# Kernel optimization log

Measured on AMD Instinct MI355X. Metric: run time of the kernel, lower is better.

## Reference

```python
import jax, jax.numpy as jnp
import numpy as np

EMB_DIM = 1024
NUM_HEADS = 16
HEAD_DIM = EMB_DIM // NUM_HEADS


def _theta_vector(head_dim):
    # theta_i = 10000^(-2i/head_dim), i = 0..head_dim/2-1 (standard RoPE)
    i = jnp.arange(head_dim // 2, dtype=jnp.float32)
    return jnp.power(10000.0, -2.0 * i / head_dim)


def _apply_rope(x, cos, sin):
    # x: [B,S,H,D]; cos,sin: [B,S,1,D/2]. Pairwise 2x2 rotation per dim-pair.
    B, S, H, D = x.shape
    xp = x.reshape(B, S, H, D // 2, 2)
    x0, x1 = xp[..., 0], xp[..., 1]
    r0 = x0 * cos - x1 * sin
    r1 = x0 * sin + x1 * cos
    return jnp.stack([r0, r1], axis=-1).reshape(B, S, H, D)


def setup_inputs() -> dict:
    key = jax.random.key(0)
    ks = jax.random.split(key, 11)
    B, S = 2, 2048
    sc = 1.0 / np.sqrt(EMB_DIM)
    x = jax.random.normal(ks[0], (B, S, EMB_DIM), dtype=jnp.float32)
    positions = jnp.sort(jax.random.randint(ks[1], (B, S), 0, 8192), axis=-1)
    Wq = jax.random.normal(ks[2], (EMB_DIM, EMB_DIM), dtype=jnp.float32) * sc
    bq = jax.random.normal(ks[3], (EMB_DIM,), dtype=jnp.float32) * 0.01
    Wk = jax.random.normal(ks[4], (EMB_DIM, EMB_DIM), dtype=jnp.float32) * sc
    bk = jax.random.normal(ks[5], (EMB_DIM,), dtype=jnp.float32) * 0.01
    Wv = jax.random.normal(ks[6], (EMB_DIM, EMB_DIM), dtype=jnp.float32) * sc
    bv = jax.random.normal(ks[7], (EMB_DIM,), dtype=jnp.float32) * 0.01
    Wo = jax.random.normal(ks[8], (EMB_DIM, EMB_DIM), dtype=jnp.float32) * sc
    bo = jax.random.normal(ks[9], (EMB_DIM,), dtype=jnp.float32) * 0.01
    return {"x": x, "positions": positions, "Wq": Wq, "bq": bq, "Wk": Wk,
            "bk": bk, "Wv": Wv, "bv": bv, "Wo": Wo, "bo": bo}


def reference(x, positions, Wq, bq, Wk, bk, Wv, bv, Wo, bo):
    B, S, E = x.shape
    H, D = NUM_HEADS, HEAD_DIM
    Q = (x @ Wq + bq).reshape(B, S, H, D)
    K = (x @ Wk + bk).reshape(B, S, H, D)
    V = (x @ Wv + bv).reshape(B, S, H, D)
    theta = _theta_vector(D)                       # [D/2]
    ang = positions.astype(jnp.float32)[..., None] * theta  # [B,S,D/2]
    cos = jnp.cos(ang)[:, :, None, :]              # [B,S,1,D/2]
    sin = jnp.sin(ang)[:, :, None, :]
    Qr = _apply_rope(Q, cos, sin).transpose(0, 2, 1, 3)   # [B,H,S,D]
    Kr = _apply_rope(K, cos, sin).transpose(0, 2, 1, 3)
    Vh = V.transpose(0, 2, 1, 3)
    scores = jnp.einsum('bhqd,bhkd->bhqk', Qr, Kr) / jnp.sqrt(jnp.float32(D))
    probs = jax.nn.softmax(scores, axis=-1)
    ctx = jnp.einsum('bhqk,bhkd->bhqd', probs, Vh)
    ctx = ctx.transpose(0, 2, 1, 3).reshape(B, S, E)
    return ctx @ Wo + bo
```

## Files before the change

kernel.cpp:

```cpp
#include <hip/hip_runtime.h>
#include <hip/hip_bf16.h>
#include <math.h>

#define B_ 2
#define S_ 2048
#define E_ 1024
#define H_ 16
#define D_ 64
#define M_ 4096
#define NT2 32
#define KVB 64

typedef __bf16 bf16;
typedef __bf16 bf16x4 __attribute__((ext_vector_type(4)));
typedef __bf16 bf16x8 __attribute__((ext_vector_type(8)));
typedef float f32x4 __attribute__((ext_vector_type(4)));
typedef float f32x16 __attribute__((ext_vector_type(16)));

__device__ __forceinline__ void gload_lds16(const void* g, void* lds) {
  __builtin_amdgcn_global_load_lds(
      (const __attribute__((address_space(1))) unsigned int*)g,
      (__attribute__((address_space(3))) unsigned int*)lds, 16, 0, 0);
}

#define MFMA16(a, b, c) __builtin_amdgcn_mfma_f32_16x16x32_bf16(a, b, c, 0, 0, 0)
#define MFMA32(a, b, c) __builtin_amdgcn_mfma_f32_32x32x16_bf16(a, b, c, 0, 0, 0)

__global__ __launch_bounds__(256)
void split_f32_kernel(const float* __restrict__ in, bf16* __restrict__ hi,
                      bf16* __restrict__ lo, int n4) {
  int i = blockIdx.x * 256 + threadIdx.x;
  if (i >= n4) return;
  float4 v = ((const float4*)in)[i];
  bf16 h0 = (bf16)v.x, h1 = (bf16)v.y, h2 = (bf16)v.z, h3 = (bf16)v.w;
  bf16x4 hv = {h0, h1, h2, h3};
  bf16x4 lv = {(bf16)(v.x - (float)h0), (bf16)(v.y - (float)h1),
               (bf16)(v.z - (float)h2), (bf16)(v.w - (float)h3)};
  *(bf16x4*)(hi + 4 * (size_t)i) = hv;
  *(bf16x4*)(lo + 4 * (size_t)i) = lv;
}

__global__ __launch_bounds__(256)
void transpose_split4_kernel(const float* __restrict__ Wq, const float* __restrict__ Wk,
                             const float* __restrict__ Wv, const float* __restrict__ Wo,
                             bf16* __restrict__ Tqh, bf16* __restrict__ Tql,
                             bf16* __restrict__ Tkh, bf16* __restrict__ Tkl,
                             bf16* __restrict__ Tvh, bf16* __restrict__ Tvl,
                             bf16* __restrict__ Toh, bf16* __restrict__ Tol) {
  const int z = blockIdx.z;
  const float* W = z == 0 ? Wq : z == 1 ? Wk : z == 2 ? Wv : Wo;
  bf16* Th = z == 0 ? Tqh : z == 1 ? Tkh : z == 2 ? Tvh : Toh;
  bf16* Tl = z == 0 ? Tql : z == 1 ? Tkl : z == 2 ? Tvl : Tol;
  __shared__ float tile[32][33];
  const int tx = threadIdx.x & 31, ty = threadIdx.x >> 5;
  const int c0 = blockIdx.x * 32, r0 = blockIdx.y * 32;
#pragma unroll
  for (int i = 0; i < 4; ++i)
    tile[ty + 8 * i][tx] = W[(size_t)(r0 + ty + 8 * i) * E_ + c0 + tx];
  __syncthreads();
#pragma unroll
  for (int i = 0; i < 4; ++i) {
    int rr = ty + 8 * i;
    float v = tile[tx][rr];
    bf16 hv = (bf16)v;
    size_t oidx = (size_t)(c0 + rr) * E_ + r0 + tx;
    Th[oidx] = hv;
    Tl[oidx] = (bf16)(v - (float)hv);
  }
}

__global__ __launch_bounds__(256)
void rope_tab_kernel(const int* __restrict__ pos, float* __restrict__ cosT,
                     float* __restrict__ sinT) {
  int idx = blockIdx.x * 256 + threadIdx.x;
  int t = idx & 31, bs = idx >> 5;
  double th = pow(10000.0, -(double)(2 * t) / 64.0);
  float ang = (float)pos[bs] * (float)th;
  double a = (double)ang;
  cosT[idx] = (float)cos(a);
  sinT[idx] = (float)sin(a);
}

#define BMg 128
#define BNg 128
#define BKg 32

__global__ __launch_bounds__(512, 4)
void gemm_qkv_kernel(const bf16* __restrict__ Ah_g, const bf16* __restrict__ Al_g,
                     const bf16* __restrict__ BhQ, const bf16* __restrict__ BlQ,
                     const bf16* __restrict__ BhK, const bf16* __restrict__ BlK,
                     const bf16* __restrict__ BhV, const bf16* __restrict__ BlV,
                     const float* __restrict__ bqp, const float* __restrict__ bkp,
                     const float* __restrict__ bvp,
                     const float* __restrict__ cosT, const float* __restrict__ sinT,
                     bf16* __restrict__ Qh, bf16* __restrict__ Qlo,
                     bf16* __restrict__ Kh, bf16* __restrict__ Klo,
                     bf16* __restrict__ VTb) {
  __shared__ bf16 lA[BMg * 64];
  __shared__ bf16 lB[BNg * 64];
  const int tid = threadIdx.x;
  const int nb = blockIdx.x;
  const int third = nb >> 3;
  const int n0 = (nb & 7) * BNg;
  const int m0 = blockIdx.y * BMg;
  const bf16* Bh_g = third == 0 ? BhQ : third == 1 ? BhK : BhV;
  const bf16* Bl_g = third == 0 ? BlQ : third == 1 ? BlK : BlV;
  const float* bias = third == 0 ? bqp : third == 1 ? bkp : bvp;
  const int wave = tid >> 6, lane = tid & 63;
  const int wr = wave >> 2, wc = wave & 3;
  const int r = lane & 31, half = lane >> 5;
  const int KD = 1024;

  f32x16 acc[2] = {};

  for (int kt = 0; kt < KD / BKg; ++kt) {
    const int k0 = kt * BKg;
    {
#pragma unroll
      for (int i = 0; i < 2; ++i) {
        int c = i * 512 + tid;
        int row = c >> 3, u = c & 7;
        int us = u ^ (row & 7);
        int uu = us & 3;
        char* lpA = (char*)lA + (size_t)(i * 512 + wave * 64) * 16;
        char* lpB = (char*)lB + (size_t)(i * 512 + wave * 64) * 16;
        const bf16* sA = (us < 4) ? Ah_g : Al_g;
        const bf16* sB = (us < 4) ? Bh_g : Bl_g;
        gload_lds16((const char*)(sA + (size_t)(m0 + row) * KD + k0) + uu * 16,
                    lpA);
        gload_lds16((const char*)(sB + (size_t)(n0 + row) * KD + k0) + uu * 16,
                    lpB);
      }
    }
    __syncthreads();
#pragma unroll
    for (int ks = 0; ks < 2; ++ks) {
      bf16x8 a_h[2], a_l[2], b_h, b_l;
#pragma unroll
      for (int mi = 0; mi < 2; ++mi) {
        int row = wr * 64 + mi * 32 + r;
        int sw = (row & 7) << 4;
        const char* base = (const char*)lA + row * 128;
        a_h[mi] = *(const bf16x8*)(base + ((ks * 32 + half * 16) ^ sw));
        a_l[mi] = *(const bf16x8*)(base + ((64 + ks * 32 + half * 16) ^ sw));
      }
      {
        int row = wc * 32 + r;
        int sw = (row & 7) << 4;
        const char* base = (const char*)lB + row * 128;
        b_h = *(const bf16x8*)(base + ((ks * 32 + half * 16) ^ sw));
        b_l = *(const bf16x8*)(base + ((64 + ks * 32 + half * 16) ^ sw));
      }
      __builtin_amdgcn_s_setprio(1);
#pragma unroll
      for (int mi = 0; mi < 2; ++mi) {
        acc[mi] = MFMA32(a_h[mi], b_h, acc[mi]);
        acc[mi] = MFMA32(a_h[mi], b_l, acc[mi]);
        acc[mi] = MFMA32(a_l[mi], b_h, acc[mi]);
      }
      __builtin_amdgcn_s_setprio(0);
    }
    __syncthreads();
  }

#pragma unroll
  for (int mi = 0; mi < 2; ++mi) {
    const int gcol = n0 + wc * 32 + r;
    const float bv = bias[gcol];
    if (third < 2) {
      bf16* outH = third == 0 ? Qh : Kh;
      bf16* outL = third == 0 ? Qlo : Klo;
      const int h = gcol >> 6, d = gcol & 63, tt = d >> 1;
#pragma unroll
      for (int tq = 0; tq < 4; ++tq) {
#pragma unroll
        for (int u = 0; u < 4; ++u) {
          int reg = tq * 4 + u;
          int grow = m0 + wr * 64 + mi * 32 + (u + 8 * tq + 4 * half);
          int s = grow & (S_ - 1), b = grow >> 11;
          float v = acc[mi][reg] + bv;
          float other = __shfl_xor(v, 1);
          float cs = cosT[(size_t)(b * S_ + s) * NT2 + tt];
          float sn = sinT[(size_t)(b * S_ + s) * NT2 + tt];
          float vr = (d & 1) ? (other * sn + v * cs) : (v * cs - other * sn);
          if (third == 0) vr *= 0.125f;
          bf16 hv = (bf16)vr;
          bf16 lv = (bf16)(vr - (float)hv);
          size_t idx = (((size_t)(b * H_ + h)) * S_ + s) * D_ + d;
          outH[idx] = hv;
          outL[idx] = lv;
        }
      }
    } else {
      const int h = gcol >> 6, d = gcol & 63;
#pragma unroll
      for (int tq = 0; tq < 4; ++tq) {
        int grow = m0 + wr * 64 + mi * 32 + (8 * tq + 4 * half);
        int s = grow & (S_ - 1), b = grow >> 11;
        ushort4 pk;
        unsigned short* pp = (unsigned short*)&pk;
#pragma unroll
        for (int u = 0; u < 4; ++u) {
          float v = acc[mi][tq * 4 + u] + bv;
          bf16 hv = (bf16)v;
          pp[u] = __builtin_bit_cast(unsigned short, hv);
        }
        *(ushort4*)((unsigned short*)VTb +
                    (((size_t)(b * H_ + h)) * D_ + d) * S_ + s) = pk;
      }
    }
  }
}

__global__ __launch_bounds__(512, 4)
void gemm_o_kernel(const bf16* __restrict__ Ah_g, const bf16* __restrict__ Al_g,
                   const bf16* __restrict__ Bh_g, const bf16* __restrict__ Bl_g,
                   const float* __restrict__ bias, float* __restrict__ outF) {
  __shared__ bf16 lA[BMg * 64];
  __shared__ bf16 lB[BNg * 64];
  const int tid = threadIdx.x;
  const int m0 = blockIdx.y * BMg, n0 = blockIdx.x * BNg;
  const int wave = tid >> 6, lane = tid & 63;
  const int wr = wave >> 2, wc = wave & 3;
  const int r = lane & 31, half = lane >> 5;
  const int KD = 1024;

  f32x16 acc[2] = {};

  for (int kt = 0; kt < KD / BKg; ++kt) {
    const int k0 = kt * BKg;
    {
#pragma unroll
      for (int i = 0; i < 2; ++i) {
        int c = i * 512 + tid;
        int row = c >> 3, u = c & 7;
        int us = u ^ (row & 7);
        int uu = us & 3;
        char* lpA = (char*)lA + (size_t)(i * 512 + wave * 64) * 16;
        char* lpB = (char*)lB + (size_t)(i * 512 + wave * 64) * 16;
        const bf16* sA = (us < 4) ? Ah_g : Al_g;
        const bf16* sB = (us < 4) ? Bh_g : Bl_g;
        gload_lds16((const char*)(sA + (size_t)(m0 + row) * KD + k0) + uu * 16,
                    lpA);
        gload_lds16((const char*)(sB + (size_t)(n0 + row) * KD + k0) + uu * 16,
                    lpB);
      }
    }
    __syncthreads();
#pragma unroll
    for (int ks = 0; ks < 2; ++ks) {
      bf16x8 a_h[2], a_l[2], b_h, b_l;
#pragma unroll
      for (int mi = 0; mi < 2; ++mi) {
        int row = wr * 64 + mi * 32 + r;
        int sw = (row & 7) << 4;
        const char* base = (const char*)lA + row * 128;
        a_h[mi] = *(const bf16x8*)(base + ((ks * 32 + half * 16) ^ sw));
        a_l[mi] = *(const bf16x8*)(base + ((64 + ks * 32 + half * 16) ^ sw));
      }
      {
        int row = wc * 32 + r;
        int sw = (row & 7) << 4;
        const char* base = (const char*)lB + row * 128;
        b_h = *(const bf16x8*)(base + ((ks * 32 + half * 16) ^ sw));
        b_l = *(const bf16x8*)(base + ((64 + ks * 32 + half * 16) ^ sw));
      }
      __builtin_amdgcn_s_setprio(1);
#pragma unroll
      for (int mi = 0; mi < 2; ++mi) {
        acc[mi] = MFMA32(a_h[mi], b_h, acc[mi]);
        acc[mi] = MFMA32(a_h[mi], b_l, acc[mi]);
        acc[mi] = MFMA32(a_l[mi], b_h, acc[mi]);
      }
      __builtin_amdgcn_s_setprio(0);
    }
    __syncthreads();
  }

#pragma unroll
  for (int mi = 0; mi < 2; ++mi) {
    const int gcol = n0 + wc * 32 + r;
    const float bv = bias[gcol];
#pragma unroll
    for (int tq = 0; tq < 4; ++tq)
#pragma unroll
      for (int u = 0; u < 4; ++u) {
        int grow = m0 + wr * 64 + mi * 32 + (u + 8 * tq + 4 * half);
        outF[(size_t)grow * E_ + gcol] = acc[mi][tq * 4 + u] + bv;
      }
  }
}

__global__ __launch_bounds__(256)
void attn_kernel(const bf16* __restrict__ Qh, const bf16* __restrict__ Ql,
                 const bf16* __restrict__ Kh, const bf16* __restrict__ Kl,
                 const bf16* __restrict__ VT, bf16* __restrict__ Ch,
                 bf16* __restrict__ Cl) {
  __shared__ bf16 sKh[2][KVB * 64];
  __shared__ bf16 sKl[2][KVB * 64];
  __shared__ bf16 sV[2][KVB * 64];

  const int tid = threadIdx.x;
  const int wave = tid >> 6, lane = tid & 63;
  const int r = lane & 15, hq = lane >> 4;
  const int bid = blockIdx.x;
  const int swz = (bid & 7) * 64 + (bid >> 3);
  const int bh = swz >> 4, qblk = swz & 15;
  const int q0 = qblk * 128 + wave * 32;
  const size_t hb = (size_t)bh * (S_ * D_);
  const size_t vb = (size_t)bh * (D_ * S_);

  bf16x8 qh[2][2], ql[2][2];
#pragma unroll
  for (int mi = 0; mi < 2; ++mi)
#pragma unroll
    for (int ks = 0; ks < 2; ++ks) {
      size_t off = hb + (size_t)(q0 + mi * 16 + r) * D_ + ks * 32 + hq * 8;
      qh[mi][ks] = *(const bf16x8*)&Qh[off];
      ql[mi][ks] = *(const bf16x8*)&Ql[off];
    }

  float m_lane[2] = {-1e30f, -1e30f};
  float l_lane[2] = {0.f, 0.f};
  f32x4 o[2][4] = {};

  auto stageK = [&](int kt, int buf) {
    const bf16* kbh = Kh + hb + (size_t)kt * (KVB * D_);
    const bf16* kbl = Kl + hb + (size_t)kt * (KVB * D_);
#pragma unroll
    for (int i = 0; i < 2; ++i) {
      int c = i * 256 + tid;
      int ldo = (i * 256 + wave * 64) * 16;
      int cs = c ^ ((c >> 3) & 7);
      gload_lds16(kbh + cs * 8, (char*)&sKh[buf][0] + ldo);
      gload_lds16(kbl + cs * 8, (char*)&sKl[buf][0] + ldo);
    }
  };
  uint4 vld[2];
  auto loadV = [&](int kt) {
    const bf16* vbp = VT + vb + kt * KVB;
#pragma unroll
    for (int i = 0; i < 2; ++i) {
      int c = i * 256 + tid;
      int row = c >> 3, w = c & 7;
      vld[i] = *(const uint4*)(vbp + (size_t)row * S_ + w * 8);
    }
  };
  auto writeV = [&](int buf) {
#pragma unroll
    for (int i = 0; i < 2; ++i) {
      int c = i * 256 + tid;
      int row = c >> 3, w = c & 7;
      int pb0 = (w >> 2) * 32 + (w & 1) * 16 + ((w >> 1) & 1) * 4;
      char* base = (char*)&sV[buf][0] + row * 128;
      uint2 lo = {vld[i].x, vld[i].y};
      uint2 hi = {vld[i].z, vld[i].w};
      *(uint2*)(base + ((pb0 * 2) ^ ((row & 7) << 4))) = lo;
      *(uint2*)(base + (((pb0 + 8) * 2) ^ ((row & 7) << 4))) = hi;
    }
  };

  stageK(0, 0);
  loadV(0);
  writeV(0);
  __syncthreads();
  int cur = 0;

  for (int kt = 0; kt < S_ / KVB; ++kt) {
    if (kt + 1 < S_ / KVB) {
      stageK(kt + 1, cur ^ 1);
      loadV(kt + 1);
    }

    f32x4 sf[2][4] = {};
#pragma unroll
    for (int nf = 0; nf < 4; ++nf)
#pragma unroll
      for (int ks = 0; ks < 2; ++ks) {
        int kk = nf * 16 + r;
        int boff = (kk * 128 + ks * 64 + hq * 16) ^ ((kk & 7) << 4);
        bf16x8 kkh = *(const bf16x8*)((const char*)&sKh[cur][0] + boff);
        bf16x8 kkl = *(const bf16x8*)((const char*)&sKl[cur][0] + boff);
#pragma unroll
        for (int mi = 0; mi < 2; ++mi) {
          sf[mi][nf] = MFMA16(kkh, qh[mi][ks], sf[mi][nf]);
          sf[mi][nf] = MFMA16(kkh, ql[mi][ks], sf[mi][nf]);
          sf[mi][nf] = MFMA16(kkl, qh[mi][ks], sf[mi][nf]);
        }
      }

    float lmax[2];
#pragma unroll
    for (int mi = 0; mi < 2; ++mi) {
      f32x4 m4;
#pragma unroll
      for (int e = 0; e < 4; ++e)
        m4[e] = fmaxf(fmaxf(sf[mi][0][e], sf[mi][1][e]),
                      fmaxf(sf[mi][2][e], sf[mi][3][e]));
      lmax[mi] = fmaxf(fmaxf(m4[0], m4[1]), fmaxf(m4[2], m4[3]));
    }
    int need = (lmax[0] > m_lane[0] + 8.f) || (lmax[1] > m_lane[1] + 8.f);
    if (__any(need)) {
#pragma unroll
      for (int mi = 0; mi < 2; ++mi) {
        float mx = lmax[mi];
        mx = fmaxf(mx, __shfl_xor(mx, 16));
        mx = fmaxf(mx, __shfl_xor(mx, 32));
        float mn = fmaxf(m_lane[mi], mx);
        float al = __expf(m_lane[mi] - mn);
        l_lane[mi] *= al;
        m_lane[mi] = mn;
        int alb = __builtin_bit_cast(int, al);
#pragma unroll
        for (int j = 0; j < 4; ++j) {
          int g = __builtin_amdgcn_ds_bpermute((hq * 4 + j) * 4, alb);
          float a = __builtin_bit_cast(float, g);
#pragma unroll
          for (int nd = 0; nd < 4; ++nd) o[mi][nd][j] *= a;
        }
      }
    }
    bf16x8 pa[2][2];
#pragma unroll
    for (int mi = 0; mi < 2; ++mi) {
      f32x4 s4 = {};
#pragma unroll
      for (int nf = 0; nf < 4; ++nf)
#pragma unroll
        for (int e = 0; e < 4; ++e) {
          float pv = __expf(sf[mi][nf][e] - m_lane[mi]);
          sf[mi][nf][e] = pv;
          s4[e] += pv;
        }
      l_lane[mi] += s4[0] + s4[1] + s4[2] + s4[3];
#pragma unroll
      for (int ks = 0; ks < 2; ++ks) {
        bf16x8 t;
#pragma unroll
        for (int e = 0; e < 4; ++e) {
          t[e] = (bf16)sf[mi][2 * ks][e];
          t[4 + e] = (bf16)sf[mi][2 * ks + 1][e];
        }
        pa[mi][ks] = t;
      }
    }

#pragma unroll
    for (int nd = 0; nd < 4; ++nd)
#pragma unroll
      for (int ks = 0; ks < 2; ++ks) {
        int dd = nd * 16 + r;
        int boff = (dd * 128 + ks * 64 + hq * 16) ^ ((dd & 7) << 4);
        bf16x8 vv = *(const bf16x8*)((const char*)&sV[cur][0] + boff);
#pragma unroll
        for (int mi = 0; mi < 2; ++mi)
          o[mi][nd] = MFMA16(pa[mi][ks], vv, o[mi][nd]);
      }

    if (kt + 1 < S_ / KVB) writeV(cur ^ 1);
    __syncthreads();
    cur ^= 1;
  }

  const int b = bh >> 4, h = bh & 15;
  float lq[2][4];
#pragma unroll
  for (int mi = 0; mi < 2; ++mi) {
    float lr = l_lane[mi];
    lr += __shfl_xor(lr, 16);
    lr += __shfl_xor(lr, 32);
    int lb = __builtin_bit_cast(int, lr);
#pragma unroll
    for (int j = 0; j < 4; ++j) {
      int g = __builtin_amdgcn_ds_bpermute((hq * 4 + j) * 4, lb);
      lq[mi][j] = __builtin_bit_cast(float, g);
    }
  }
#pragma unroll
  for (int mi = 0; mi < 2; ++mi)
#pragma unroll
    for (int nd = 0; nd < 4; ++nd)
#pragma unroll
      for (int j = 0; j < 4; ++j) {
        int s = q0 + mi * 16 + hq * 4 + j;
        int d = nd * 16 + r;
        float ov = o[mi][nd][j] / lq[mi][j];
        bf16 hv = (bf16)ov;
        bf16 lv = (bf16)(ov - (float)hv);
        size_t idx = (((size_t)(b * S_ + s)) * H_ + h) * D_ + d;
        Ch[idx] = hv;
        Cl[idx] = lv;
      }
}

extern "C" void kernel_launch(void* const* d_in, const int* in_sizes, int n_in,
                              void* d_out, int out_size, void* d_ws, size_t ws_size,
                              hipStream_t stream) {
  const float* x = (const float*)d_in[0];
  const int* pos = (const int*)d_in[1];
  const float* Wq = (const float*)d_in[2];
  const float* bq = (const float*)d_in[3];
  const float* Wk = (const float*)d_in[4];
  const float* bk = (const float*)d_in[5];
  const float* Wv = (const float*)d_in[6];
  const float* bv = (const float*)d_in[7];
  const float* Wo = (const float*)d_in[8];
  const float* bo = (const float*)d_in[9];
  float* out = (float*)d_out;

  char* p = (char*)d_ws;
  auto alloc = [&](size_t bytes) {
    char* rp = p;
    p += (bytes + 255) & ~(size_t)255;
    return rp;
  };
  const size_t XB = (size_t)M_ * E_ * sizeof(bf16);
  const size_t WB = (size_t)E_ * E_ * sizeof(bf16);
  const size_t TB = (size_t)B_ * S_ * NT2 * sizeof(float);
  bf16* Xh = (bf16*)alloc(XB);
  bf16* Xl = (bf16*)alloc(XB);
  bf16* WqTh = (bf16*)alloc(WB); bf16* WqTl = (bf16*)alloc(WB);
  bf16* WkTh = (bf16*)alloc(WB); bf16* WkTl = (bf16*)alloc(WB);
  bf16* WvTh = (bf16*)alloc(WB); bf16* WvTl = (bf16*)alloc(WB);
  bf16* WoTh = (bf16*)alloc(WB); bf16* WoTl = (bf16*)alloc(WB);
  float* cosT = (float*)alloc(TB);
  float* sinT = (float*)alloc(TB);
  bf16* Qh = (bf16*)alloc(XB); bf16* Qlo = (bf16*)alloc(XB);
  bf16* Kh = (bf16*)alloc(XB); bf16* Klo = (bf16*)alloc(XB);
  bf16* VTb = (bf16*)alloc(XB);
  bf16* Ch = Xh;
  bf16* Cl = Xl;

  split_f32_kernel<<<M_ * E_ / 4 / 256, 256, 0, stream>>>(x, Xh, Xl, M_ * E_ / 4);
  dim3 tg(32, 32, 4);
  transpose_split4_kernel<<<tg, 256, 0, stream>>>(Wq, Wk, Wv, Wo, WqTh, WqTl,
                                                  WkTh, WkTl, WvTh, WvTl, WoTh,
                                                  WoTl);
  rope_tab_kernel<<<B_ * S_ * NT2 / 256, 256, 0, stream>>>(pos, cosT, sinT);

  dim3 gq(24, 32);
  gemm_qkv_kernel<<<gq, 512, 0, stream>>>(Xh, Xl, WqTh, WqTl, WkTh, WkTl, WvTh,
                                          WvTl, bq, bk, bv, cosT, sinT, Qh, Qlo,
                                          Kh, Klo, VTb);

  attn_kernel<<<B_ * H_ * (S_ / 128), 256, 0, stream>>>(Qh, Qlo, Kh, Klo, VTb,
                                                        Ch, Cl);

  dim3 go(8, 32);
  gemm_o_kernel<<<go, 512, 0, stream>>>(Ch, Cl, WoTh, WoTl, bo, out);
}
```

Measured before the change: 237.7 us.

## Merge prep kernels, split MFMA accumulators, retile output projection GEMM

Fuses the x split, weight transpose/split and RoPE table kernels into a single launch with block-range dispatch, which removes two kernel launches and their gaps. In both GEMMs the low-part correction MFMA now accumulates into a second accumulator, which breaks the serial dependency chain so consecutive MFMAs can issue back to back. The output projection GEMM moves to 64x128 tiles with 256 threads and twice as many blocks, improving occupancy across CUs. This costs extra accumulator registers and changes the summation order slightly.

```diff
diff --git a/kernel.cpp b/kernel.cpp
--- a/kernel.cpp
+++ b/kernel.cpp
@@ -27,58 +27,57 @@
 #define MFMA32(a, b, c) __builtin_amdgcn_mfma_f32_32x32x16_bf16(a, b, c, 0, 0, 0)
 
 __global__ __launch_bounds__(256)
-void split_f32_kernel(const float* __restrict__ in, bf16* __restrict__ hi,
-                      bf16* __restrict__ lo, int n4) {
-  int i = blockIdx.x * 256 + threadIdx.x;
-  if (i >= n4) return;
-  float4 v = ((const float4*)in)[i];
-  bf16 h0 = (bf16)v.x, h1 = (bf16)v.y, h2 = (bf16)v.z, h3 = (bf16)v.w;
-  bf16x4 hv = {h0, h1, h2, h3};
-  bf16x4 lv = {(bf16)(v.x - (float)h0), (bf16)(v.y - (float)h1),
-               (bf16)(v.z - (float)h2), (bf16)(v.w - (float)h3)};
-  *(bf16x4*)(hi + 4 * (size_t)i) = hv;
-  *(bf16x4*)(lo + 4 * (size_t)i) = lv;
-}
-
-__global__ __launch_bounds__(256)
-void transpose_split4_kernel(const float* __restrict__ Wq, const float* __restrict__ Wk,
-                             const float* __restrict__ Wv, const float* __restrict__ Wo,
-                             bf16* __restrict__ Tqh, bf16* __restrict__ Tql,
-                             bf16* __restrict__ Tkh, bf16* __restrict__ Tkl,
-                             bf16* __restrict__ Tvh, bf16* __restrict__ Tvl,
-                             bf16* __restrict__ Toh, bf16* __restrict__ Tol) {
-  const int z = blockIdx.z;
-  const float* W = z == 0 ? Wq : z == 1 ? Wk : z == 2 ? Wv : Wo;
-  bf16* Th = z == 0 ? Tqh : z == 1 ? Tkh : z == 2 ? Tvh : Toh;
-  bf16* Tl = z == 0 ? Tql : z == 1 ? Tkl : z == 2 ? Tvl : Tol;
-  __shared__ float tile[32][33];
-  const int tx = threadIdx.x & 31, ty = threadIdx.x >> 5;
-  const int c0 = blockIdx.x * 32, r0 = blockIdx.y * 32;
-#pragma unroll
-  for (int i = 0; i < 4; ++i)
-    tile[ty + 8 * i][tx] = W[(size_t)(r0 + ty + 8 * i) * E_ + c0 + tx];
-  __syncthreads();
-#pragma unroll
-  for (int i = 0; i < 4; ++i) {
-    int rr = ty + 8 * i;
-    float v = tile[tx][rr];
-    bf16 hv = (bf16)v;
-    size_t oidx = (size_t)(c0 + rr) * E_ + r0 + tx;
-    Th[oidx] = hv;
-    Tl[oidx] = (bf16)(v - (float)hv);
-  }
-}
-
-__global__ __launch_bounds__(256)
-void rope_tab_kernel(const int* __restrict__ pos, float* __restrict__ cosT,
-                     float* __restrict__ sinT) {
-  int idx = blockIdx.x * 256 + threadIdx.x;
-  int t = idx & 31, bs = idx >> 5;
-  double th = pow(10000.0, -(double)(2 * t) / 64.0);
-  float ang = (float)pos[bs] * (float)th;
-  double a = (double)ang;
-  cosT[idx] = (float)cos(a);
-  sinT[idx] = (float)sin(a);
+void prep_kernel(const float* __restrict__ x, const int* __restrict__ pos,
+                 const float* __restrict__ Wq, const float* __restrict__ Wk,
+                 const float* __restrict__ Wv, const float* __restrict__ Wo,
+                 bf16* __restrict__ Xh, bf16* __restrict__ Xl,
+                 bf16* __restrict__ Tqh, bf16* __restrict__ Tql,
+                 bf16* __restrict__ Tkh, bf16* __restrict__ Tkl,
+                 bf16* __restrict__ Tvh, bf16* __restrict__ Tvl,
+                 bf16* __restrict__ Toh, bf16* __restrict__ Tol,
+                 float* __restrict__ cosT, float* __restrict__ sinT) {
+  const int bid = blockIdx.x;
+  if (bid < 4096) {
+    int i = bid * 256 + threadIdx.x;
+    float4 v = ((const float4*)x)[i];
+    bf16 h0 = (bf16)v.x, h1 = (bf16)v.y, h2 = (bf16)v.z, h3 = (bf16)v.w;
+    bf16x4 hv = {h0, h1, h2, h3};
+    bf16x4 lv = {(bf16)(v.x - (float)h0), (bf16)(v.y - (float)h1),
+                 (bf16)(v.z - (float)h2), (bf16)(v.w - (float)h3)};
+    *(bf16x4*)(Xh + 4 * (size_t)i) = hv;
+    *(bf16x4*)(Xl + 4 * (size_t)i) = lv;
+  } else if (bid < 8192) {
+    int t = bid - 4096;
+    int z = t >> 10, rem = t & 1023;
+    int bx = rem & 31, by = rem >> 5;
+    const float* W = z == 0 ? Wq : z == 1 ? Wk : z == 2 ? Wv : Wo;
+    bf16* Th = z == 0 ? Tqh : z == 1 ? Tkh : z == 2 ? Tvh : Toh;
+    bf16* Tl = z == 0 ? Tql : z == 1 ? Tkl : z == 2 ? Tvl : Tol;
+    __shared__ float tile[32][33];
+    const int tx = threadIdx.x & 31, ty = threadIdx.x >> 5;
+    const int c0 = bx * 32, r0 = by * 32;
+#pragma unroll
+    for (int i = 0; i < 4; ++i)
+      tile[ty + 8 * i][tx] = W[(size_t)(r0 + ty + 8 * i) * E_ + c0 + tx];
+    __syncthreads();
+#pragma unroll
+    for (int i = 0; i < 4; ++i) {
+      int rr = ty + 8 * i;
+      float v = tile[tx][rr];
+      bf16 hv = (bf16)v;
+      size_t oidx = (size_t)(c0 + rr) * E_ + r0 + tx;
+      Th[oidx] = hv;
+      Tl[oidx] = (bf16)(v - (float)hv);
+    }
+  } else {
+    int idx = (bid - 8192) * 256 + threadIdx.x;
+    int t = idx & 31, bs = idx >> 5;
+    double th = pow(10000.0, -(double)(2 * t) / 64.0);
+    float ang = (float)pos[bs] * (float)th;
+    double a = (double)ang;
+    cosT[idx] = (float)cos(a);
+    sinT[idx] = (float)sin(a);
+  }
 }
 
 #define BMg 128
@@ -112,6 +111,7 @@
   const int KD = 1024;
 
   f32x16 acc[2] = {};
+  f32x16 acc2[2] = {};
 
   for (int kt = 0; kt < KD / BKg; ++kt) {
     const int k0 = kt * BKg;
@@ -156,7 +156,7 @@
       for (int mi = 0; mi < 2; ++mi) {
         acc[mi] = MFMA32(a_h[mi], b_h, acc[mi]);
         acc[mi] = MFMA32(a_h[mi], b_l, acc[mi]);
-        acc[mi] = MFMA32(a_l[mi], b_h, acc[mi]);
+        acc2[mi] = MFMA32(a_l[mi], b_h, acc2[mi]);
       }
       __builtin_amdgcn_s_setprio(0);
     }
@@ -178,7 +178,7 @@
           int reg = tq * 4 + u;
           int grow = m0 + wr * 64 + mi * 32 + (u + 8 * tq + 4 * half);
           int s = grow & (S_ - 1), b = grow >> 11;
-          float v = acc[mi][reg] + bv;
+          float v = acc[mi][reg] + acc2[mi][reg] + bv;
           float other = __shfl_xor(v, 1);
           float cs = cosT[(size_t)(b * S_ + s) * NT2 + tt];
           float sn = sinT[(size_t)(b * S_ + s) * NT2 + tt];
@@ -201,7 +201,7 @@
         unsigned short* pp = (unsigned short*)&pk;
 #pragma unroll
         for (int u = 0; u < 4; ++u) {
-          float v = acc[mi][tq * 4 + u] + bv;
+          float v = acc[mi][tq * 4 + u] + acc2[mi][tq * 4 + u] + bv;
           bf16 hv = (bf16)v;
           pp[u] = __builtin_bit_cast(unsigned short, hv);
         }
@@ -212,65 +212,76 @@
   }
 }
 
-__global__ __launch_bounds__(512, 4)
+#define BMo 64
+#define BNo 128
+
+__global__ __launch_bounds__(256, 4)
 void gemm_o_kernel(const bf16* __restrict__ Ah_g, const bf16* __restrict__ Al_g,
                    const bf16* __restrict__ Bh_g, const bf16* __restrict__ Bl_g,
                    const float* __restrict__ bias, float* __restrict__ outF) {
-  __shared__ bf16 lA[BMg * 64];
-  __shared__ bf16 lB[BNg * 64];
+  __shared__ bf16 lA[BMo * 64];
+  __shared__ bf16 lB[BNo * 64];
   const int tid = threadIdx.x;
-  const int m0 = blockIdx.y * BMg, n0 = blockIdx.x * BNg;
+  const int n0 = blockIdx.x * BNo, m0 = blockIdx.y * BMo;
   const int wave = tid >> 6, lane = tid & 63;
-  const int wr = wave >> 2, wc = wave & 3;
+  const int wr = wave >> 1, wc = wave & 1;
   const int r = lane & 31, half = lane >> 5;
   const int KD = 1024;
 
   f32x16 acc[2] = {};
+  f32x16 acc2[2] = {};
 
   for (int kt = 0; kt < KD / BKg; ++kt) {
     const int k0 = kt * BKg;
     {
 #pragma unroll
-      for (int i = 0; i < 2; ++i) {
-        int c = i * 512 + tid;
-        int row = c >> 3, u = c & 7;
-        int us = u ^ (row & 7);
-        int uu = us & 3;
-        char* lpA = (char*)lA + (size_t)(i * 512 + wave * 64) * 16;
-        char* lpB = (char*)lB + (size_t)(i * 512 + wave * 64) * 16;
-        const bf16* sA = (us < 4) ? Ah_g : Al_g;
-        const bf16* sB = (us < 4) ? Bh_g : Bl_g;
-        gload_lds16((const char*)(sA + (size_t)(m0 + row) * KD + k0) + uu * 16,
-                    lpA);
-        gload_lds16((const char*)(sB + (size_t)(n0 + row) * KD + k0) + uu * 16,
-                    lpB);
+      for (int i = 0; i < 6; ++i) {
+        int c = i * 256 + tid;
+        if (i < 2) {
+          int row = c >> 3, u = c & 7;
+          int us = u ^ (row & 7);
+          const bf16* sA = (us < 4) ? Ah_g : Al_g;
+          char* lp = (char*)lA + (size_t)(i * 256 + wave * 64) * 16;
+          gload_lds16((const char*)(sA + (size_t)(m0 + row) * KD + k0) +
+                          (us & 3) * 16,
+                      lp);
+        } else {
+          int cb = c - 512;
+          int row = cb >> 3, u = cb & 7;
+          int us = u ^ (row & 7);
+          const bf16* sB = (us < 4) ? Bh_g : Bl_g;
+          char* lp = (char*)lB + (size_t)((i - 2) * 256 + wave * 64) * 16;
+          gload_lds16((const char*)(sB + (size_t)(n0 + row) * KD + k0) +
+                          (us & 3) * 16,
+                      lp);
+        }
       }
     }
     __syncthreads();
 #pragma unroll
     for (int ks = 0; ks < 2; ++ks) {
-      bf16x8 a_h[2], a_l[2], b_h, b_l;
-#pragma unroll
-      for (int mi = 0; mi < 2; ++mi) {
-        int row = wr * 64 + mi * 32 + r;
+      bf16x8 a_h, a_l, b_h[2], b_l[2];
+      {
+        int row = wr * 32 + r;
         int sw = (row & 7) << 4;
         const char* base = (const char*)lA + row * 128;
-        a_h[mi] = *(const bf16x8*)(base + ((ks * 32 + half * 16) ^ sw));
-        a_l[mi] = *(const bf16x8*)(base + ((64 + ks * 32 + half * 16) ^ sw));
-      }
-      {
-        int row = wc * 32 + r;
+        a_h = *(const bf16x8*)(base + ((ks * 32 + half * 16) ^ sw));
+        a_l = *(const bf16x8*)(base + ((64 + ks * 32 + half * 16) ^ sw));
+      }
+#pragma unroll
+      for (int ni = 0; ni < 2; ++ni) {
+        int row = wc * 64 + ni * 32 + r;
         int sw = (row & 7) << 4;
         const char* base = (const char*)lB + row * 128;
-        b_h = *(const bf16x8*)(base + ((ks * 32 + half * 16) ^ sw));
-        b_l = *(const bf16x8*)(base + ((64 + ks * 32 + half * 16) ^ sw));
+        b_h[ni] = *(const bf16x8*)(base + ((ks * 32 + half * 16) ^ sw));
+        b_l[ni] = *(const bf16x8*)(base + ((64 + ks * 32 + half * 16) ^ sw));
       }
       __builtin_amdgcn_s_setprio(1);
 #pragma unroll
-      for (int mi = 0; mi < 2; ++mi) {
-        acc[mi] = MFMA32(a_h[mi], b_h, acc[mi]);
-        acc[mi] = MFMA32(a_h[mi], b_l, acc[mi]);
-        acc[mi] = MFMA32(a_l[mi], b_h, acc[mi]);
+      for (int ni = 0; ni < 2; ++ni) {
+        acc[ni] = MFMA32(a_h, b_h[ni], acc[ni]);
+        acc[ni] = MFMA32(a_h, b_l[ni], acc[ni]);
+        acc2[ni] = MFMA32(a_l, b_h[ni], acc2[ni]);
       }
       __builtin_amdgcn_s_setprio(0);
     }
@@ -278,15 +289,16 @@
   }
 
 #pragma unroll
-  for (int mi = 0; mi < 2; ++mi) {
-    const int gcol = n0 + wc * 32 + r;
+  for (int ni = 0; ni < 2; ++ni) {
+    const int gcol = n0 + wc * 64 + ni * 32 + r;
     const float bv = bias[gcol];
 #pragma unroll
     for (int tq = 0; tq < 4; ++tq)
 #pragma unroll
       for (int u = 0; u < 4; ++u) {
-        int grow = m0 + wr * 64 + mi * 32 + (u + 8 * tq + 4 * half);
-        outF[(size_t)grow * E_ + gcol] = acc[mi][tq * 4 + u] + bv;
+        int grow = m0 + wr * 32 + (u + 8 * tq + 4 * half);
+        outF[(size_t)grow * E_ + gcol] =
+            acc[ni][tq * 4 + u] + acc2[ni][tq * 4 + u] + bv;
       }
   }
 }
@@ -531,12 +543,9 @@
   bf16* Ch = Xh;
   bf16* Cl = Xl;
 
-  split_f32_kernel<<<M_ * E_ / 4 / 256, 256, 0, stream>>>(x, Xh, Xl, M_ * E_ / 4);
-  dim3 tg(32, 32, 4);
-  transpose_split4_kernel<<<tg, 256, 0, stream>>>(Wq, Wk, Wv, Wo, WqTh, WqTl,
-                                                  WkTh, WkTl, WvTh, WvTl, WoTh,
-                                                  WoTl);
-  rope_tab_kernel<<<B_ * S_ * NT2 / 256, 256, 0, stream>>>(pos, cosT, sinT);
+  prep_kernel<<<8704, 256, 0, stream>>>(x, pos, Wq, Wk, Wv, Wo, Xh, Xl, WqTh,
+                                        WqTl, WkTh, WkTl, WvTh, WvTl, WoTh,
+                                        WoTl, cosT, sinT);
 
   dim3 gq(24, 32);
   gemm_qkv_kernel<<<gq, 512, 0, stream>>>(Xh, Xl, WqTh, WqTl, WkTh, WkTl, WvTh,
@@ -546,6 +555,6 @@
   attn_kernel<<<B_ * H_ * (S_ / 128), 256, 0, stream>>>(Qh, Qlo, Kh, Klo, VTb,
                                                         Ch, Cl);
 
-  dim3 go(8, 32);
-  gemm_o_kernel<<<go, 512, 0, stream>>>(Ch, Cl, WoTh, WoTl, bo, out);
+  dim3 go(8, 64);
+  gemm_o_kernel<<<go, 256, 0, stream>>>(Ch, Cl, WoTh, WoTl, bo, out);
 }
```

Result: faster. 228.7 us (-3.8%).
